# Performance work log

Hardware: AMD Instinct MI355X
Metric: run time of the kernel (lower is better)

## Reference

```python
import jax, jax.numpy as jnp
import numpy as np

N_NODES = 50000
N_EDGES = 800000
HIDDEN = 128
NUM_LAYERS = 3
NEG_SLOPE = 0.2  # PyG GATConv default leaky_relu slope


def setup_inputs() -> dict:
    key = jax.random.key(0)
    ks = jax.random.split(key, 10)
    d = HIDDEN
    glorot = 1.0 / np.sqrt(d)
    inp = {
        "x": jax.random.normal(ks[0], (N_NODES, d), dtype=jnp.float32),
        "edge_index": jax.random.randint(ks[1], (2, N_EDGES), 0, N_NODES, dtype=jnp.int32),
        "edge_mask": jax.random.uniform(ks[2], (N_EDGES,), dtype=jnp.float32),
        # GATConv params (heads=1)
        "W_gat": jax.random.normal(ks[3], (d, d), dtype=jnp.float32) * glorot,
        "a_src": jax.random.normal(ks[4], (d,), dtype=jnp.float32) * glorot,
        "a_dst": jax.random.normal(ks[5], (d,), dtype=jnp.float32) * glorot,
        "b_gat": jnp.zeros((d,), dtype=jnp.float32),
        # Stacked GCNConv params
        "W_gcn": jax.random.normal(ks[6], (NUM_LAYERS, d, d), dtype=jnp.float32) * glorot,
        "b_gcn": jnp.zeros((NUM_LAYERS, d), dtype=jnp.float32),
    }
    return inp


def _seg_softmax(e, seg, n):
    m = jax.ops.segment_max(e, seg, num_segments=n)
    p = jnp.exp(e - m[seg])
    s = jax.ops.segment_sum(p, seg, num_segments=n)
    return p / s[seg]


def reference(x, edge_index, edge_mask, W_gat, a_src, a_dst, b_gat, W_gcn, b_gcn):
    N = x.shape[0]
    loops = jnp.arange(N, dtype=edge_index.dtype)
    src = jnp.concatenate([edge_index[0], loops])  # [E+N] with self loops
    dst = jnp.concatenate([edge_index[1], loops])

    # --- GATConv (heads=1, add_self_loops=True); edge_attr ignored (edge_dim=None) ---
    xp = x @ W_gat                                      # [N, d]
    e = jax.nn.leaky_relu((xp @ a_src)[src] + (xp @ a_dst)[dst], NEG_SLOPE)
    alpha = _seg_softmax(e, dst, N)                     # segment softmax over incoming edges
    h = jax.ops.segment_sum(alpha[:, None] * xp[src], dst, num_segments=N) + b_gat

    # --- GCN normalization with edge_mask as edge_weight (self-loop weight = 1) ---
    w = jnp.concatenate([edge_mask, jnp.ones((N,), dtype=edge_mask.dtype)])
    deg = jax.ops.segment_sum(w, dst, num_segments=N)
    dinv = jnp.where(deg > 0, jax.lax.rsqrt(jnp.maximum(deg, 1e-12)), 0.0)
    norm = dinv[src] * w * dinv[dst]                    # [E+N]

    outs = [h]
    for l in range(NUM_LAYERS):
        z = outs[-1] @ W_gcn[l]                         # [N, d]
        z = jax.ops.segment_sum(norm[:, None] * z[src], dst, num_segments=N) + b_gcn[l]
        outs.append(jax.nn.relu(z))

    # JumpingKnowledge 'max': elementwise max over layer outputs
    return jnp.max(jnp.stack(outs, axis=0), axis=0)
```

## Files before the change

### kernel.cpp

```cpp
#include <hip/hip_runtime.h>

#define HIDDEN 128
#define NEG_SLOPE 0.2f
#define P_SORT 256

typedef unsigned short ushort_t;
typedef __attribute__((ext_vector_type(8))) short short8;
typedef __attribute__((ext_vector_type(4))) float floatx4;

static inline size_t align_up(size_t x, size_t a){ return (x + a - 1) & ~(a - 1); }

__device__ __forceinline__ ushort_t f2b(float f){
  unsigned u = __float_as_uint(f);
  unsigned r = (u + 0x7FFFu + ((u >> 16) & 1u)) >> 16;
  return (ushort_t)r;
}

__device__ __forceinline__ void fma8(float* acc, uint4 v, float a){
  acc[0] += a * __uint_as_float(v.x << 16);
  acc[1] += a * __uint_as_float(v.x & 0xFFFF0000u);
  acc[2] += a * __uint_as_float(v.y << 16);
  acc[3] += a * __uint_as_float(v.y & 0xFFFF0000u);
  acc[4] += a * __uint_as_float(v.z << 16);
  acc[5] += a * __uint_as_float(v.z & 0xFFFF0000u);
  acc[6] += a * __uint_as_float(v.w << 16);
  acc[7] += a * __uint_as_float(v.w & 0xFFFF0000u);
}

__device__ __forceinline__ uint4 pack8(const float* f){
  uint4 u;
  u.x = (unsigned)f2b(f[0]) | ((unsigned)f2b(f[1]) << 16);
  u.y = (unsigned)f2b(f[2]) | ((unsigned)f2b(f[3]) << 16);
  u.z = (unsigned)f2b(f[4]) | ((unsigned)f2b(f[5]) << 16);
  u.w = (unsigned)f2b(f[6]) | ((unsigned)f2b(f[7]) << 16);
  return u;
}


__global__ __launch_bounds__(256) void k_b1cnt(const int* __restrict__ dst,
                                               int* __restrict__ bcnt,
                                               int E, int epb, int nbkt){
  __shared__ unsigned c[256];
  int t = threadIdx.x;
  c[t] = 0;
  __syncthreads();
  int e0 = blockIdx.x * epb;
  int e1 = min(E, e0 + epb);
  for (int e = e0 + t; e < e1; e += 256) atomicAdd(&c[dst[e] >> 8], 1u);
  __syncthreads();
  if (t < nbkt) bcnt[t * P_SORT + blockIdx.x] = (int)c[t];
}

__global__ void k_scan1(const int* __restrict__ in, int* __restrict__ incl,
                        int* __restrict__ blockSums, int M){
  __shared__ int sd[256];
  int t = threadIdx.x;
  int i = blockIdx.x*256 + t;
  int v = (i < M) ? in[i] : 0;
  sd[t] = v; __syncthreads();
  for (int off = 1; off < 256; off <<= 1){
    int add = (t >= off) ? sd[t-off] : 0;
    __syncthreads();
    sd[t] += add;
    __syncthreads();
  }
  if (i < M) incl[i] = sd[t];
  if (t == 255) blockSums[blockIdx.x] = sd[255];
}

__global__ void k_scan2(const int* __restrict__ blockSums, int* __restrict__ blockOffs, int nb){
  __shared__ int sd[256];
  __shared__ int carry;
  int t = threadIdx.x;
  if (t == 0) carry = 0;
  __syncthreads();
  for (int base = 0; base < nb; base += 256){
    int i = base + t;
    int v = (i < nb) ? blockSums[i] : 0;
    sd[t] = v; __syncthreads();
    for (int off = 1; off < 256; off <<= 1){
      int add = (t >= off) ? sd[t-off] : 0;
      __syncthreads();
      sd[t] += add;
      __syncthreads();
    }
    if (i < nb) blockOffs[i] = carry + sd[t] - v;
    __syncthreads();
    if (t == 0) carry += sd[255];
    __syncthreads();
  }
}

__global__ void k_scanex(int* __restrict__ arr, const int* __restrict__ in,
                         const int* __restrict__ blockOffs, int M){
  int i = blockIdx.x*256 + threadIdx.x;
  if (i < M) arr[i] = arr[i] - in[i] + blockOffs[blockIdx.x];
}

__global__ __launch_bounds__(256) void k_b1place(const int* __restrict__ src,
                                                 const int* __restrict__ dst,
                                                 const float* __restrict__ w,
                                                 const int* __restrict__ ebase,
                                                 unsigned* __restrict__ tpk,
                                                 float* __restrict__ tw,
                                                 int E, int epb){
  __shared__ unsigned c[256];
  int t = threadIdx.x;
  c[t] = 0;
  __syncthreads();
  int e0 = blockIdx.x * epb;
  int e1 = min(E, e0 + epb);
  for (int e = e0 + t; e < e1; e += 256){
    int d = dst[e];
    int b = d >> 8;
    unsigned r = atomicAdd(&c[b], 1u);
    int pos = ebase[b * P_SORT + blockIdx.x] + (int)r;
    tpk[pos] = (unsigned)src[e] | ((unsigned)(d & 255) << 16);
    tw[pos]  = w[e];
  }
}

__global__ __launch_bounds__(256) void k_b2(const unsigned* __restrict__ tpk,
                                            const float* __restrict__ tw,
                                            const int* __restrict__ ebase,
                                            int* __restrict__ col_src,
                                            float* __restrict__ col_w,
                                            int* __restrict__ rowp,
                                            float* __restrict__ dinv,
                                            int N, int E, int nbkt){
  __shared__ unsigned hcnt[256];
  __shared__ int sd[256];
  __shared__ int lofs[256];
  __shared__ unsigned rcnt[256];
  __shared__ float wsum[256];
  int b = blockIdx.x, t = threadIdx.x;
  int e0 = ebase[b * P_SORT];
  int e1 = (b + 1 < nbkt) ? ebase[(b + 1) * P_SORT] : E;
  hcnt[t] = 0; rcnt[t] = 0; wsum[t] = 0.f;
  __syncthreads();
  for (int e = e0 + t; e < e1; e += 256) atomicAdd(&hcnt[(tpk[e] >> 16) & 255u], 1u);
  __syncthreads();
  int v = (int)hcnt[t];
  sd[t] = v; __syncthreads();
  for (int off = 1; off < 256; off <<= 1){
    int add = (t >= off) ? sd[t-off] : 0;
    __syncthreads();
    sd[t] += add;
    __syncthreads();
  }
  lofs[t] = sd[t] - v;
  int node = b*256 + t;
  if (node < N) rowp[node] = e0 + sd[t] - v;
  if (b == 0 && t == 0) rowp[N] = E;
  __syncthreads();
  for (int e = e0 + t; e < e1; e += 256){
    unsigned pk = tpk[e];
    float wv = tw[e];
    unsigned dl = (pk >> 16) & 255u;
    unsigned r = atomicAdd(&rcnt[dl], 1u);
    int pos = e0 + lofs[dl] + (int)r;
    col_src[pos] = (int)(pk & 0xFFFFu);
    col_w[pos]   = wv;
    atomicAdd(&wsum[dl], wv);
  }
  __syncthreads();
  if (node < N) dinv[node] = rsqrtf(wsum[t] + 1.0f);
}


__global__ void k_cast_x(const float* __restrict__ x, unsigned* __restrict__ xb, long n2){
  long i = (long)blockIdx.x*256 + threadIdx.x;
  if (i >= n2) return;
  float2 v = ((const float2*)x)[i];
  xb[i] = (unsigned)f2b(v.x) | ((unsigned)f2b(v.y) << 16);
}

__global__ void k_cast_w(const float* __restrict__ Wg, const float* __restrict__ Wc,
                         ushort_t* __restrict__ Wt){
  int i = blockIdx.x*256 + threadIdx.x;
  int mat = i >> 14, idx = i & 16383;
  int k = idx >> 7, n = idx & 127;
  float v = (mat == 0) ? Wg[idx] : Wc[(mat-1)*16384 + idx];
  Wt[mat*16384 + n*128 + k] = f2b(v);
}

template<int DOTS>
__global__ __launch_bounds__(256) void k_gemm(const ushort_t* __restrict__ A,
                                              const ushort_t* __restrict__ Wt,
                                              ushort_t* __restrict__ C,
                                              const float* __restrict__ a_src,
                                              const float* __restrict__ a_dst,
                                              const float* __restrict__ dinv,
                                              float2* __restrict__ attr,
                                              float* __restrict__ sdst, int M){
  int wave = threadIdx.x >> 6, l = threadIdx.x & 63;
  int q = l >> 4, lm = l & 15;
  int rowBase = blockIdx.x*128 + wave*32;
  floatx4 acc[2][8];
  #pragma unroll
  for (int mt = 0; mt < 2; mt++)
    #pragma unroll
    for (int nt = 0; nt < 8; nt++) acc[mt][nt] = (floatx4){0.f,0.f,0.f,0.f};

  #pragma unroll
  for (int kc = 0; kc < 4; kc++){
    int k0 = kc*32 + q*8;
    short8 a[2];
    #pragma unroll
    for (int mt = 0; mt < 2; mt++){
      long r = rowBase + mt*16 + lm;
      if (r < M) a[mt] = *(const short8*)(A + r*128 + k0);
      else       a[mt] = (short8){0,0,0,0,0,0,0,0};
    }
    #pragma unroll
    for (int nt = 0; nt < 8; nt++){
      short8 b = *(const short8*)(Wt + (nt*16 + lm)*128 + k0);
      acc[0][nt] = __builtin_amdgcn_mfma_f32_16x16x32_bf16(a[0], b, acc[0][nt], 0, 0, 0);
      acc[1][nt] = __builtin_amdgcn_mfma_f32_16x16x32_bf16(a[1], b, acc[1][nt], 0, 0, 0);
    }
  }
  #pragma unroll
  for (int mt = 0; mt < 2; mt++){
    #pragma unroll
    for (int r = 0; r < 4; r++){
      long row = rowBase + mt*16 + q*4 + r;
      if (row < M){
        #pragma unroll
        for (int nt = 0; nt < 8; nt++)
          C[row*128 + nt*16 + lm] = f2b(acc[mt][nt][r]);
      }
    }
  }
  if (DOTS){
    float as8[8], ad8[8];
    #pragma unroll
    for (int nt = 0; nt < 8; nt++){ as8[nt] = a_src[nt*16 + lm]; ad8[nt] = a_dst[nt*16 + lm]; }
    #pragma unroll
    for (int mt = 0; mt < 2; mt++){
      #pragma unroll
      for (int r = 0; r < 4; r++){
        float ps = 0.f, pd = 0.f;
        #pragma unroll
        for (int nt = 0; nt < 8; nt++){
          ps += acc[mt][nt][r] * as8[nt];
          pd += acc[mt][nt][r] * ad8[nt];
        }
        #pragma unroll
        for (int off = 1; off <= 8; off <<= 1){
          ps += __shfl_xor(ps, off, 64);
          pd += __shfl_xor(pd, off, 64);
        }
        long row = rowBase + mt*16 + q*4 + r;
        if (lm == 0 && row < M){
          attr[row] = make_float2(ps, dinv[row]);
          sdst[row] = pd;
        }
      }
    }
  }
}

__global__ void k_post(const int* __restrict__ rowp, const int* __restrict__ col_src,
                       const float* __restrict__ col_w, const float2* __restrict__ attr,
                       const float* __restrict__ sdst, const float* __restrict__ dinv,
                       int2* __restrict__ col_en, int2* __restrict__ col_ea,
                       float2* __restrict__ nparm, int N){
  int n = blockIdx.x*4 + (threadIdx.x >> 6);
  int l = threadIdx.x & 63;
  if (n >= N) return;
  int rs = rowp[n], re = rowp[n+1];
  float dn = dinv[n], sdd = sdst[n];
  float es = attr[n].x + sdd;
  es = (es >= 0.f) ? es : NEG_SLOPE*es;
  float pself = __expf(es);
  float ps = 0.f;
  for (int j = rs + l; j < re; j += 64){
    int s = col_src[j];
    float w = col_w[j];
    float2 a = attr[s];
    col_en[j] = make_int2(s, __float_as_int(a.y * w * dn));
    float ee = a.x + sdd;
    ee = (ee >= 0.f) ? ee : NEG_SLOPE*ee;
    float pe = __expf(ee);
    ps += pe;
    col_ea[j] = make_int2(s, __float_as_int(pe));
  }
  #pragma unroll
  for (int off = 32; off >= 1; off >>= 1) ps += __shfl_xor(ps, off, 64);
  if (l == 0){
    float inv = 1.f / (ps + pself);
    nparm[n] = make_float2(inv, pself * inv);
  }
}

template<int MODE>
__global__ __launch_bounds__(256) void k_agg(const ushort_t* __restrict__ feat,
                                             const int* __restrict__ rowp,
                                             const int2* __restrict__ col,
                                             const float2* __restrict__ np,
                                             const float* __restrict__ dinv,
                                             const float* __restrict__ bias,
                                             ushort_t* __restrict__ out,
                                             float* __restrict__ y, int N){
  int n = blockIdx.x*4 + (threadIdx.x >> 6);
  if (n >= N) return;
  int l = threadIdx.x & 63;
  int sub = l >> 4, q = l & 15;
  int rs = rowp[n], re = rowp[n+1];
  const uint4* f16 = (const uint4*)feat;
  float acc[8] = {0.f,0.f,0.f,0.f,0.f,0.f,0.f,0.f};
  for (int base = rs; base < re; base += 16){
    int2 p[4]; float a[4];
    #pragma unroll
    for (int j = 0; j < 4; j++){
      int e = base + sub + 4*j;
      int cc = min(e, re-1);
      p[j] = col[cc];
      a[j] = (e < re) ? __int_as_float(p[j].y) : 0.f;
    }
    uint4 v[4];
    #pragma unroll
    for (int j = 0; j < 4; j++) v[j] = f16[(size_t)p[j].x*16 + q];
    #pragma unroll
    for (int j = 0; j < 4; j++) fma8(acc, v[j], a[j]);
  }
  #pragma unroll
  for (int j = 0; j < 8; j++){
    acc[j] += __shfl_xor(acc[j], 16, 64);
    acc[j] += __shfl_xor(acc[j], 32, 64);
  }
  if (sub == 0){
    float sc;
    if (MODE == 0){
      float2 pp = np[n];
      #pragma unroll
      for (int j = 0; j < 8; j++) acc[j] *= pp.x;
      sc = pp.y;
    } else {
      float di = dinv[n];
      sc = di * di;
    }
    uint4 v = f16[(size_t)n*16 + q];
    fma8(acc, v, sc);
    float4 b0 = ((const float4*)bias)[q*2];
    float4 b1 = ((const float4*)bias)[q*2 + 1];
    acc[0]+=b0.x; acc[1]+=b0.y; acc[2]+=b0.z; acc[3]+=b0.w;
    acc[4]+=b1.x; acc[5]+=b1.y; acc[6]+=b1.z; acc[7]+=b1.w;
    if (MODE == 1){
      #pragma unroll
      for (int j = 0; j < 8; j++) acc[j] = fmaxf(acc[j], 0.f);
    }
    ((uint4*)out)[(size_t)n*16 + q] = pack8(acc);
    float4* y4 = (float4*)y;
    size_t yi = (size_t)n*32 + q*2;
    float4 n0 = make_float4(acc[0], acc[1], acc[2], acc[3]);
    float4 n1 = make_float4(acc[4], acc[5], acc[6], acc[7]);
    if (MODE == 0){
      y4[yi] = n0; y4[yi+1] = n1;
    } else {
      float4 y0 = y4[yi], y1 = y4[yi+1];
      y0.x=fmaxf(y0.x,n0.x); y0.y=fmaxf(y0.y,n0.y); y0.z=fmaxf(y0.z,n0.z); y0.w=fmaxf(y0.w,n0.w);
      y1.x=fmaxf(y1.x,n1.x); y1.y=fmaxf(y1.y,n1.y); y1.z=fmaxf(y1.z,n1.z); y1.w=fmaxf(y1.w,n1.w);
      y4[yi] = y0; y4[yi+1] = y1;
    }
  }
}

extern "C" void kernel_launch(void* const* d_in, const int* in_sizes, int n_in,
                              void* d_out, int out_size, void* d_ws, size_t ws_size,
                              hipStream_t stream){
  const float* x      = (const float*)d_in[0];
  const int*   eidx   = (const int*)d_in[1];
  const float* emask  = (const float*)d_in[2];
  const float* W_gat  = (const float*)d_in[3];
  const float* a_src  = (const float*)d_in[4];
  const float* a_dst  = (const float*)d_in[5];
  const float* b_gat  = (const float*)d_in[6];
  const float* W_gcn  = (const float*)d_in[7];
  const float* b_gcn  = (const float*)d_in[8];
  int N = in_sizes[0] / HIDDEN;
  int E = in_sizes[1] / 2;
  const int* src = eidx;
  const int* dst = eidx + E;

  char* p = (char*)d_ws;
  auto carve = [&](size_t bytes)->char*{ char* q = p; p += align_up(bytes, 512); return q; };
  ushort_t* xb   = (ushort_t*)carve((size_t)N*HIDDEN*2);
  ushort_t* zb   = (ushort_t*)carve((size_t)N*HIDDEN*2);
  ushort_t* hb   = (ushort_t*)carve((size_t)N*HIDDEN*2);
  ushort_t* Wt   = (ushort_t*)carve((size_t)4*HIDDEN*HIDDEN*2);
  float2* attr   = (float2*)carve((size_t)N*8);
  float2* nparm  = (float2*)carve((size_t)N*8);
  float* sdst    = (float*)carve((size_t)N*4);
  float* dinv    = (float*)carve((size_t)N*4);
  int*   rowp    = (int*)  carve((size_t)(N+1)*4);
  int*   col_src = (int*)  carve((size_t)E*4);
  float* col_w   = (float*)carve((size_t)E*4);
  int2*  col_en  = (int2*) carve((size_t)E*8);
  int2*  col_ea  = (int2*) carve((size_t)E*8);
  unsigned* tpk  = (unsigned*)carve((size_t)E*4);
  float* tw      = (float*)carve((size_t)E*4);
  int nbkt = (N + 255) >> 8;
  int M    = nbkt * P_SORT;
  int*   bcnt  = (int*)carve((size_t)M*4);
  int*   ebase = (int*)carve((size_t)M*4);
  int nbs = (M + 255) / 256;
  int*   blockSums = (int*)carve((size_t)nbs*4);
  int*   blockOffs = (int*)carve((size_t)nbs*4);
  (void)ws_size; (void)n_in; (void)out_size;

  int epb = (E + P_SORT - 1) / P_SORT;
  int gb  = (N + 127) / 128;
  int nwb = (N + 3) / 4;
  long n2 = (long)N*64;
  int cb  = (int)((n2 + 255) / 256);

  k_b1cnt  <<<P_SORT, 256, 0, stream>>>(dst, bcnt, E, epb, nbkt);
  k_scan1  <<<nbs, 256, 0, stream>>>(bcnt, ebase, blockSums, M);
  k_scan2  <<<1,   256, 0, stream>>>(blockSums, blockOffs, nbs);
  k_scanex <<<nbs, 256, 0, stream>>>(ebase, bcnt, blockOffs, M);
  k_b1place<<<P_SORT, 256, 0, stream>>>(src, dst, emask, ebase, tpk, tw, E, epb);
  k_b2     <<<nbkt, 256, 0, stream>>>(tpk, tw, ebase, col_src, col_w, rowp, dinv, N, E, nbkt);

  k_cast_x<<<cb, 256, 0, stream>>>(x, (unsigned*)xb, n2);
  k_cast_w<<<(4*HIDDEN*HIDDEN)/256, 256, 0, stream>>>(W_gat, W_gcn, Wt);

  k_gemm<1><<<gb, 256, 0, stream>>>(xb, Wt, zb, a_src, a_dst, dinv, attr, sdst, N);
  k_post<<<nwb, 256, 0, stream>>>(rowp, col_src, col_w, attr, sdst, dinv,
                                  col_en, col_ea, nparm, N);

  k_agg<0><<<nwb, 256, 0, stream>>>(zb, rowp, col_ea, nparm, dinv,
                                    b_gat, hb, (float*)d_out, N);
  for (int l = 0; l < 3; l++){
    k_gemm<0><<<gb, 256, 0, stream>>>(hb, Wt + (size_t)(l+1)*HIDDEN*HIDDEN, zb,
                                      a_src, a_dst, dinv, attr, sdst, N);
    k_agg<1><<<nwb, 256, 0, stream>>>(zb, rowp, col_en, nparm, dinv,
                                      b_gcn + (size_t)l*HIDDEN, hb, (float*)d_out, N);
  }
}
```

Before: 360.1 us.

## Defer JK max to bf16 final kernel, pack CSR arrays, narrow post lanes

Stores each layer's output as a separate bf16 buffer and computes the JumpingKnowledge max in one final kernel, removing the per-layer fp32 read-modify-write of the output. Packs source index and edge weight into int2 arrays for the bucket sort and CSR. Maps k_post to 16 lanes per node to match the average degree, and unrolls aggregation to 6 edges per iteration. This costs more workspace, and the max is now taken over bf16-rounded values rather than fp32.

After: 350.5 us. 2.7% less time.

```diff
diff --git a/kernel.cpp b/kernel.cpp
--- a/kernel.cpp
+++ b/kernel.cpp
@@ -101,8 +101,7 @@
                                                  const int* __restrict__ dst,
                                                  const float* __restrict__ w,
                                                  const int* __restrict__ ebase,
-                                                 unsigned* __restrict__ tpk,
-                                                 float* __restrict__ tw,
+                                                 int2* __restrict__ tpw,
                                                  int E, int epb){
   __shared__ unsigned c[256];
   int t = threadIdx.x;
@@ -115,16 +114,14 @@
     int b = d >> 8;
     unsigned r = atomicAdd(&c[b], 1u);
     int pos = ebase[b * P_SORT + blockIdx.x] + (int)r;
-    tpk[pos] = (unsigned)src[e] | ((unsigned)(d & 255) << 16);
-    tw[pos]  = w[e];
-  }
-}
-
-__global__ __launch_bounds__(256) void k_b2(const unsigned* __restrict__ tpk,
-                                            const float* __restrict__ tw,
+    tpw[pos] = make_int2((int)((unsigned)src[e] | ((unsigned)(d & 255) << 16)),
+                         __float_as_int(w[e]));
+  }
+}
+
+__global__ __launch_bounds__(256) void k_b2(const int2* __restrict__ tpw,
                                             const int* __restrict__ ebase,
-                                            int* __restrict__ col_src,
-                                            float* __restrict__ col_w,
+                                            int2* __restrict__ col_sw,
                                             int* __restrict__ rowp,
                                             float* __restrict__ dinv,
                                             int N, int E, int nbkt){
@@ -138,7 +135,8 @@
   int e1 = (b + 1 < nbkt) ? ebase[(b + 1) * P_SORT] : E;
   hcnt[t] = 0; rcnt[t] = 0; wsum[t] = 0.f;
   __syncthreads();
-  for (int e = e0 + t; e < e1; e += 256) atomicAdd(&hcnt[(tpk[e] >> 16) & 255u], 1u);
+  for (int e = e0 + t; e < e1; e += 256)
+    atomicAdd(&hcnt[((unsigned)tpw[e].x >> 16) & 255u], 1u);
   __syncthreads();
   int v = (int)hcnt[t];
   sd[t] = v; __syncthreads();
@@ -154,14 +152,12 @@
   if (b == 0 && t == 0) rowp[N] = E;
   __syncthreads();
   for (int e = e0 + t; e < e1; e += 256){
-    unsigned pk = tpk[e];
-    float wv = tw[e];
-    unsigned dl = (pk >> 16) & 255u;
+    int2 pw = tpw[e];
+    unsigned dl = ((unsigned)pw.x >> 16) & 255u;
     unsigned r = atomicAdd(&rcnt[dl], 1u);
     int pos = e0 + lofs[dl] + (int)r;
-    col_src[pos] = (int)(pk & 0xFFFFu);
-    col_w[pos]   = wv;
-    atomicAdd(&wsum[dl], wv);
+    col_sw[pos] = make_int2((int)((unsigned)pw.x & 0xFFFFu), pw.y);
+    atomicAdd(&wsum[dl], __int_as_float(pw.y));
   }
   __syncthreads();
   if (node < N) dinv[node] = rsqrtf(wsum[t] + 1.0f);
@@ -260,23 +256,24 @@
   }
 }
 
-__global__ void k_post(const int* __restrict__ rowp, const int* __restrict__ col_src,
-                       const float* __restrict__ col_w, const float2* __restrict__ attr,
-                       const float* __restrict__ sdst, const float* __restrict__ dinv,
+__global__ void k_post(const int* __restrict__ rowp, const int2* __restrict__ col_sw,
+                       const float2* __restrict__ attr, const float* __restrict__ sdst,
                        int2* __restrict__ col_en, int2* __restrict__ col_ea,
                        float2* __restrict__ nparm, int N){
-  int n = blockIdx.x*4 + (threadIdx.x >> 6);
-  int l = threadIdx.x & 63;
+  int n = blockIdx.x*16 + (threadIdx.x >> 4);
+  int l = threadIdx.x & 15;
   if (n >= N) return;
   int rs = rowp[n], re = rowp[n+1];
-  float dn = dinv[n], sdd = sdst[n];
-  float es = attr[n].x + sdd;
+  float2 an = attr[n];
+  float dn = an.y, sdd = sdst[n];
+  float es = an.x + sdd;
   es = (es >= 0.f) ? es : NEG_SLOPE*es;
   float pself = __expf(es);
   float ps = 0.f;
-  for (int j = rs + l; j < re; j += 64){
-    int s = col_src[j];
-    float w = col_w[j];
+  for (int j = rs + l; j < re; j += 16){
+    int2 sw = col_sw[j];
+    int s = sw.x;
+    float w = __int_as_float(sw.y);
     float2 a = attr[s];
     col_en[j] = make_int2(s, __float_as_int(a.y * w * dn));
     float ee = a.x + sdd;
@@ -285,8 +282,8 @@
     ps += pe;
     col_ea[j] = make_int2(s, __float_as_int(pe));
   }
-  #pragma unroll
-  for (int off = 32; off >= 1; off >>= 1) ps += __shfl_xor(ps, off, 64);
+  ps += __shfl_xor(ps, 1); ps += __shfl_xor(ps, 2);
+  ps += __shfl_xor(ps, 4); ps += __shfl_xor(ps, 8);
   if (l == 0){
     float inv = 1.f / (ps + pself);
     nparm[n] = make_float2(inv, pself * inv);
@@ -300,8 +297,7 @@
                                              const float2* __restrict__ np,
                                              const float* __restrict__ dinv,
                                              const float* __restrict__ bias,
-                                             ushort_t* __restrict__ out,
-                                             float* __restrict__ y, int N){
+                                             ushort_t* __restrict__ out, int N){
   int n = blockIdx.x*4 + (threadIdx.x >> 6);
   if (n >= N) return;
   int l = threadIdx.x & 63;
@@ -309,20 +305,20 @@
   int rs = rowp[n], re = rowp[n+1];
   const uint4* f16 = (const uint4*)feat;
   float acc[8] = {0.f,0.f,0.f,0.f,0.f,0.f,0.f,0.f};
-  for (int base = rs; base < re; base += 16){
-    int2 p[4]; float a[4];
-    #pragma unroll
-    for (int j = 0; j < 4; j++){
+  for (int base = rs; base < re; base += 24){
+    int2 p[6]; float a[6];
+    #pragma unroll
+    for (int j = 0; j < 6; j++){
       int e = base + sub + 4*j;
       int cc = min(e, re-1);
       p[j] = col[cc];
       a[j] = (e < re) ? __int_as_float(p[j].y) : 0.f;
     }
-    uint4 v[4];
-    #pragma unroll
-    for (int j = 0; j < 4; j++) v[j] = f16[(size_t)p[j].x*16 + q];
-    #pragma unroll
-    for (int j = 0; j < 4; j++) fma8(acc, v[j], a[j]);
+    uint4 v[6];
+    #pragma unroll
+    for (int j = 0; j < 6; j++) v[j] = f16[(size_t)p[j].x*16 + q];
+    #pragma unroll
+    for (int j = 0; j < 6; j++) fma8(acc, v[j], a[j]);
   }
   #pragma unroll
   for (int j = 0; j < 8; j++){
@@ -351,19 +347,27 @@
       for (int j = 0; j < 8; j++) acc[j] = fmaxf(acc[j], 0.f);
     }
     ((uint4*)out)[(size_t)n*16 + q] = pack8(acc);
-    float4* y4 = (float4*)y;
-    size_t yi = (size_t)n*32 + q*2;
-    float4 n0 = make_float4(acc[0], acc[1], acc[2], acc[3]);
-    float4 n1 = make_float4(acc[4], acc[5], acc[6], acc[7]);
-    if (MODE == 0){
-      y4[yi] = n0; y4[yi+1] = n1;
-    } else {
-      float4 y0 = y4[yi], y1 = y4[yi+1];
-      y0.x=fmaxf(y0.x,n0.x); y0.y=fmaxf(y0.y,n0.y); y0.z=fmaxf(y0.z,n0.z); y0.w=fmaxf(y0.w,n0.w);
-      y1.x=fmaxf(y1.x,n1.x); y1.y=fmaxf(y1.y,n1.y); y1.z=fmaxf(y1.z,n1.z); y1.w=fmaxf(y1.w,n1.w);
-      y4[yi] = y0; y4[yi+1] = y1;
-    }
-  }
+  }
+}
+
+__global__ void k_jk(const uint4* __restrict__ h0, const uint4* __restrict__ h1,
+                     const uint4* __restrict__ h2, const uint4* __restrict__ h3,
+                     float4* __restrict__ out, long n16){
+  long i = (long)blockIdx.x*256 + threadIdx.x;
+  if (i >= n16) return;
+  uint4 a = h0[i], b = h1[i], c = h2[i], d = h3[i];
+  float m[8];
+  #pragma unroll
+  for (int j = 0; j < 4; j++){
+    unsigned ua = (&a.x)[j], ub = (&b.x)[j], uc = (&c.x)[j], ud = (&d.x)[j];
+    float lo = fmaxf(fmaxf(__uint_as_float(ua << 16), __uint_as_float(ub << 16)),
+                     fmaxf(__uint_as_float(uc << 16), __uint_as_float(ud << 16)));
+    float hi = fmaxf(fmaxf(__uint_as_float(ua & 0xFFFF0000u), __uint_as_float(ub & 0xFFFF0000u)),
+                     fmaxf(__uint_as_float(uc & 0xFFFF0000u), __uint_as_float(ud & 0xFFFF0000u)));
+    m[j*2] = lo; m[j*2+1] = hi;
+  }
+  out[i*2]   = make_float4(m[0], m[1], m[2], m[3]);
+  out[i*2+1] = make_float4(m[4], m[5], m[6], m[7]);
 }
 
 extern "C" void kernel_launch(void* const* d_in, const int* in_sizes, int n_in,
@@ -387,19 +391,20 @@
   auto carve = [&](size_t bytes)->char*{ char* q = p; p += align_up(bytes, 512); return q; };
   ushort_t* xb   = (ushort_t*)carve((size_t)N*HIDDEN*2);
   ushort_t* zb   = (ushort_t*)carve((size_t)N*HIDDEN*2);
-  ushort_t* hb   = (ushort_t*)carve((size_t)N*HIDDEN*2);
+  ushort_t* h0   = (ushort_t*)carve((size_t)N*HIDDEN*2);
+  ushort_t* h1   = (ushort_t*)carve((size_t)N*HIDDEN*2);
+  ushort_t* h2   = (ushort_t*)carve((size_t)N*HIDDEN*2);
+  ushort_t* h3   = (ushort_t*)carve((size_t)N*HIDDEN*2);
   ushort_t* Wt   = (ushort_t*)carve((size_t)4*HIDDEN*HIDDEN*2);
   float2* attr   = (float2*)carve((size_t)N*8);
   float2* nparm  = (float2*)carve((size_t)N*8);
   float* sdst    = (float*)carve((size_t)N*4);
   float* dinv    = (float*)carve((size_t)N*4);
   int*   rowp    = (int*)  carve((size_t)(N+1)*4);
-  int*   col_src = (int*)  carve((size_t)E*4);
-  float* col_w   = (float*)carve((size_t)E*4);
+  int2*  col_sw  = (int2*) carve((size_t)E*8);
   int2*  col_en  = (int2*) carve((size_t)E*8);
   int2*  col_ea  = (int2*) carve((size_t)E*8);
-  unsigned* tpk  = (unsigned*)carve((size_t)E*4);
-  float* tw      = (float*)carve((size_t)E*4);
+  int2*  tpw     = (int2*) carve((size_t)E*8);
   int nbkt = (N + 255) >> 8;
   int M    = nbkt * P_SORT;
   int*   bcnt  = (int*)carve((size_t)M*4);
@@ -412,29 +417,34 @@
   int epb = (E + P_SORT - 1) / P_SORT;
   int gb  = (N + 127) / 128;
   int nwb = (N + 3) / 4;
+  int nqb = (N + 15) / 16;
   long n2 = (long)N*64;
   int cb  = (int)((n2 + 255) / 256);
+  long n16 = (long)N*16;
+  int jb  = (int)((n16 + 255) / 256);
 
   k_b1cnt  <<<P_SORT, 256, 0, stream>>>(dst, bcnt, E, epb, nbkt);
   k_scan1  <<<nbs, 256, 0, stream>>>(bcnt, ebase, blockSums, M);
   k_scan2  <<<1,   256, 0, stream>>>(blockSums, blockOffs, nbs);
   k_scanex <<<nbs, 256, 0, stream>>>(ebase, bcnt, blockOffs, M);
-  k_b1place<<<P_SORT, 256, 0, stream>>>(src, dst, emask, ebase, tpk, tw, E, epb);
-  k_b2     <<<nbkt, 256, 0, stream>>>(tpk, tw, ebase, col_src, col_w, rowp, dinv, N, E, nbkt);
+  k_b1place<<<P_SORT, 256, 0, stream>>>(src, dst, emask, ebase, tpw, E, epb);
+  k_b2     <<<nbkt, 256, 0, stream>>>(tpw, ebase, col_sw, rowp, dinv, N, E, nbkt);
 
   k_cast_x<<<cb, 256, 0, stream>>>(x, (unsigned*)xb, n2);
   k_cast_w<<<(4*HIDDEN*HIDDEN)/256, 256, 0, stream>>>(W_gat, W_gcn, Wt);
 
   k_gemm<1><<<gb, 256, 0, stream>>>(xb, Wt, zb, a_src, a_dst, dinv, attr, sdst, N);
-  k_post<<<nwb, 256, 0, stream>>>(rowp, col_src, col_w, attr, sdst, dinv,
-                                  col_en, col_ea, nparm, N);
-
-  k_agg<0><<<nwb, 256, 0, stream>>>(zb, rowp, col_ea, nparm, dinv,
-                                    b_gat, hb, (float*)d_out, N);
+  k_post<<<nqb, 256, 0, stream>>>(rowp, col_sw, attr, sdst, col_en, col_ea, nparm, N);
+
+  k_agg<0><<<nwb, 256, 0, stream>>>(zb, rowp, col_ea, nparm, dinv, b_gat, h0, N);
+  ushort_t* hs[4] = {h0, h1, h2, h3};
   for (int l = 0; l < 3; l++){
-    k_gemm<0><<<gb, 256, 0, stream>>>(hb, Wt + (size_t)(l+1)*HIDDEN*HIDDEN, zb,
+    k_gemm<0><<<gb, 256, 0, stream>>>(hs[l], Wt + (size_t)(l+1)*HIDDEN*HIDDEN, zb,
                                       a_src, a_dst, dinv, attr, sdst, N);
     k_agg<1><<<nwb, 256, 0, stream>>>(zb, rowp, col_en, nparm, dinv,
-                                      b_gcn + (size_t)l*HIDDEN, hb, (float*)d_out, N);
-  }
-}
+                                      b_gcn + (size_t)l*HIDDEN, hs[l+1], N);
+  }
+  k_jk<<<jb, 256, 0, stream>>>((const uint4*)h0, (const uint4*)h1,
+                               (const uint4*)h2, (const uint4*)h3,
+                               (float4*)d_out, n16);
+}
```
